# Kernel optimization log

Measured on AMD Instinct MI355X. Metric: run time of the kernel, lower is better.

The kernel has to match this reference:

```python
import jax, jax.numpy as jnp
import numpy as np

D_MODEL = 1024
N_HEADS = 16
D_KV = 64
B, S = 2, 2048


def setup_inputs() -> dict:
    key = jax.random.key(0)
    ks = jax.random.split(key, 7)
    scale = 1.0 / np.sqrt(D_MODEL)
    return {
        "query": jax.random.normal(ks[0], (B, S, D_MODEL), jnp.float32),
        "key": jax.random.normal(ks[1], (B, S, D_MODEL), jnp.float32),
        "value": jax.random.normal(ks[2], (B, S, D_MODEL), jnp.float32),
        "mask": jnp.zeros((B, 1, 1, S), jnp.float32),
        "Wq": jax.random.normal(ks[3], (D_MODEL, N_HEADS * D_KV), jnp.float32) * scale,
        "Wk": jax.random.normal(ks[4], (D_MODEL, N_HEADS * D_KV), jnp.float32) * scale,
        "Wv": jax.random.normal(ks[5], (D_MODEL, N_HEADS * D_KV), jnp.float32) * scale,
        "Wo": jax.random.normal(ks[6], (N_HEADS * D_KV, D_MODEL), jnp.float32) * scale,
    }


def _split_heads(x):
    b, s, _ = x.shape
    return x.reshape(b, s, N_HEADS, D_KV).transpose(0, 2, 1, 3)  # [B,H,S,Dk]


def reference(query, key, value, mask, Wq, Wk, Wv, Wo):
    q = _split_heads(query @ Wq)
    k = _split_heads(key @ Wk)
    v = _split_heads(value @ Wv)
    scores = jnp.einsum("bhqd,bhkd->bhqk", q, k) / jnp.sqrt(
        jnp.asarray(D_KV, scores_dtype := q.dtype)
    )
    scores = scores + mask
    attn = jax.nn.softmax(scores, axis=-1)  # dropout_rate=0 -> identity
    ctx = jnp.einsum("bhqk,bhkd->bhqd", attn, v)
    ctx = ctx.transpose(0, 2, 1, 3).reshape(query.shape[0], -1, N_HEADS * D_KV)
    hidden = ctx @ Wo
    return hidden
```

## Files before the change

kernel.cpp:

```cpp
#include <hip/hip_runtime.h>
#include <hip/hip_bf16.h>
#include <stdint.h>

typedef __bf16 bf16;
typedef __bf16 bf16x8 __attribute__((ext_vector_type(8)));
typedef __bf16 bf16x4 __attribute__((ext_vector_type(4)));
typedef float  f32x4  __attribute__((ext_vector_type(4)));
typedef float  f32x16 __attribute__((ext_vector_type(16)));

#define S_LEN  2048
#define NH     16
#define DKV    64
#define DMODEL 1024
#define LOG2E  1.4426950408889634f

#define SBAR()       __builtin_amdgcn_s_barrier()
#define SFENCE()     __builtin_amdgcn_sched_barrier(0)
#define WAIT_VM(N)   asm volatile("s_waitcnt vmcnt(" #N ")" ::: "memory")
#define WAIT_LGKM0() asm volatile("s_waitcnt lgkmcnt(0)" ::: "memory")

__device__ __forceinline__ void async_load16(const void* g, void* l) {
  __builtin_amdgcn_global_load_lds(
      (const __attribute__((address_space(1))) uint32_t*)(uintptr_t)g,
      (__attribute__((address_space(3))) uint32_t*)(uintptr_t)l,
      16, 0, 0);
}

__global__ void prep(const float* __restrict__ W0, const float* __restrict__ W1,
                     const float* __restrict__ W2, const float* __restrict__ W3,
                     const float* __restrict__ Aq, const float* __restrict__ Ak,
                     const float* __restrict__ Av,
                     bf16* __restrict__ T0, bf16* __restrict__ T1,
                     bf16* __restrict__ T2, bf16* __restrict__ T3,
                     bf16* __restrict__ Qb, bf16* __restrict__ Kb, bf16* __restrict__ Vb)
{
  const int z = blockIdx.z;
  const int tid = threadIdx.x;
  if (z < 4) {
    if (blockIdx.x >= 16) return;
    const float* W = (z == 0) ? W0 : (z == 1) ? W1 : (z == 2) ? W2 : W3;
    bf16* T = (z == 0) ? T0 : (z == 1) ? T1 : (z == 2) ? T2 : T3;
    __shared__ float tile[64][65];
    int n0 = blockIdx.x * 64, k0 = blockIdx.y * 64;
    int c4 = (tid & 15) * 4;
    int rr = tid >> 4;
    for (int g = 0; g < 4; ++g) {
      int k = g * 16 + rr;
      f32x4 v = *(const f32x4*)(W + (size_t)(k0 + k) * DMODEL + n0 + c4);
      tile[k][c4] = v[0]; tile[k][c4 + 1] = v[1];
      tile[k][c4 + 2] = v[2]; tile[k][c4 + 3] = v[3];
    }
    __syncthreads();
    int kc = tid & 7, rn2 = tid >> 3;
    for (int pass = 0; pass < 2; ++pass) {
      int rn = pass * 32 + rn2;
      bf16x8 o;
      for (int w = 0; w < 8; ++w) o[w] = (bf16)tile[kc * 8 + w][rn];
      *(bf16x8*)(T + (size_t)(n0 + rn) * DMODEL + k0 + kc * 8) = o;
    }
  } else {
    const float* S = (z == 4) ? Aq : (z == 5) ? Ak : Av;
    bf16* D = (z == 4) ? Qb : (z == 5) ? Kb : Vb;
    size_t base = (((size_t)blockIdx.y * 64 + blockIdx.x) * 256 + tid) * 16;
    f32x4 v0 = *(const f32x4*)(S + base);
    f32x4 v1 = *(const f32x4*)(S + base + 4);
    f32x4 v2 = *(const f32x4*)(S + base + 8);
    f32x4 v3 = *(const f32x4*)(S + base + 12);
    bf16x8 o0, o1;
    for (int w = 0; w < 4; ++w) { o0[w] = (bf16)v0[w]; o0[w + 4] = (bf16)v1[w]; }
    for (int w = 0; w < 4; ++w) { o1[w] = (bf16)v2[w]; o1[w + 4] = (bf16)v3[w]; }
    *(bf16x8*)(D + base) = o0;
    *(bf16x8*)(D + base + 8) = o1;
  }
}

__global__ __launch_bounds__(256) void gemm_qkv(
    const bf16* __restrict__ Aq, const bf16* __restrict__ Ak, const bf16* __restrict__ Av,
    const bf16* __restrict__ Bq, const bf16* __restrict__ Bk, const bf16* __restrict__ Bv,
    bf16* __restrict__ Cq, bf16* __restrict__ Ck, bf16* __restrict__ Cv)
{
  __shared__ __align__(16) char smem[33792];
  bf16* As = (bf16*)smem;
  bf16* Bs = (bf16*)(smem + 16384);
  bf16* Ls = (bf16*)smem;

  const int z = blockIdx.z;
  const bf16* A  = (z == 0) ? Aq : (z == 1) ? Ak : Av;
  const bf16* Bt = (z == 0) ? Bq : (z == 1) ? Bk : Bv;
  bf16* C        = (z == 0) ? Cq : (z == 1) ? Ck : Cv;

  const int m0 = blockIdx.x * 128;
  const int n0 = blockIdx.y * 128;
  const int tid = threadIdx.x;
  const int lane = tid & 63;
  const int wave = tid >> 6;
  const int wm = (wave >> 1) * 64;
  const int wn = (wave & 1) * 64;
  const int row = lane & 15;
  const int quad = lane >> 4;

  f32x4 acc[4][4];
  for (int i = 0; i < 4; ++i)
    for (int j = 0; j < 4; ++j) acc[i][j] = (f32x4){0.f, 0.f, 0.f, 0.f};

  for (int kt = 0; kt < 16; ++kt) {
    const int kk = kt << 6;
    for (int j = 0; j < 4; ++j) {
      int base = j * 256 + wave * 64;
      int idx = base + lane;
      int r = idx >> 3;
      int cc = (idx & 7) ^ (r & 7);
      async_load16(A  + (size_t)(m0 + r) * DMODEL + kk + cc * 8,
                   (char*)As + (size_t)base * 16);
      async_load16(Bt + (size_t)(n0 + r) * DMODEL + kk + cc * 8,
                   (char*)Bs + (size_t)base * 16);
    }
    WAIT_VM(0);
    SBAR();
    for (int ks = 0; ks < 2; ++ks) {
      bf16x8 af[4], bfr[4];
      for (int i = 0; i < 4; ++i) {
        int rr = wm + i * 16 + row;
        af[i] = *(const bf16x8*)(As + rr * 64 + (((quad + ks * 4) ^ (rr & 7)) << 3));
      }
      for (int j = 0; j < 4; ++j) {
        int rr = wn + j * 16 + row;
        bfr[j] = *(const bf16x8*)(Bs + rr * 64 + (((quad + ks * 4) ^ (rr & 7)) << 3));
      }
      for (int i = 0; i < 4; ++i)
        for (int j = 0; j < 4; ++j)
          acc[i][j] = __builtin_amdgcn_mfma_f32_16x16x32_bf16(af[i], bfr[j], acc[i][j], 0, 0, 0);
    }
    SBAR();
  }

  if (z != 2) {
    const int bq = m0 >> 11;
    __syncthreads();
    for (int i = 0; i < 4; ++i)
      for (int j = 0; j < 4; ++j)
        for (int r = 0; r < 4; ++r)
          Ls[(wm + i * 16 + quad * 4 + r) * 132 + wn + j * 16 + row] = (bf16)acc[i][j][r];
    __syncthreads();
    for (int u = 0; u < 8; ++u) {
      int cc = u * 256 + tid;
      int rloc = cc >> 4, c8 = (cc & 15) * 8;
      int s = (m0 + rloc) & 2047;
      int gn = n0 + c8;
      int h = gn >> 6, d = gn & 63;
      bf16x8 val = *(const bf16x8*)(Ls + rloc * 132 + c8);
      *(bf16x8*)(C + (((size_t)(bq * NH + h)) * S_LEN + s) * DKV + d) = val;
    }
  } else {
    for (int i = 0; i < 4; ++i)
      for (int j = 0; j < 4; ++j) {
        int gm = m0 + wm + i * 16 + quad * 4;
        int gn = n0 + wn + j * 16 + row;
        int b = gm >> 11, s = gm & 2047;
        int h = gn >> 6,  d = gn & 63;
        int bh = b * NH + h;
        int tile = s >> 6, kb = (s & 63) >> 2;
        int half = (kb >> 1) & 1;
        int p = (kb & 1) + ((kb >> 2) & 1) * 2 + (kb >> 3) * 4;
        bf16x4 t;
        for (int r = 0; r < 4; ++r) t[r] = (bf16)acc[i][j][r];
        *(bf16x4*)(C + ((((size_t)bh * 32 + tile) * 8 + p) * 64 + d) * 8 + half * 4) = t;
      }
  }
}

__global__ __launch_bounds__(256, 4) void attn_kernel(
    const bf16* __restrict__ Qh, const bf16* __restrict__ Kh, const bf16* __restrict__ Vperm,
    const float* __restrict__ mask, bf16* __restrict__ Opart, float* __restrict__ Lpart)
{
  __shared__ __align__(16) bf16 Ks[2][64 * 64];
  __shared__ __align__(16) bf16 Vts[2][64 * 64];
  __shared__ __align__(16) float masks2[2][64];

  const int bh = blockIdx.x;
  const int b = bh >> 4;
  const int q0 = blockIdx.y * 128;
  const int zh = blockIdx.z;
  const int tid = threadIdx.x;
  const int lane = tid & 63;
  const int wave = tid >> 6;
  const int ln = lane & 31;
  const int hi = lane >> 5;
  const float SC2 = 0.125f * LOG2E;

  const int qg = q0 + wave * 32 + ln;
  bf16x8 qf[4];
  {
    const bf16* qrow = Qh + ((size_t)bh * S_LEN + qg) * DKV;
    for (int c = 0; c < 4; ++c)
      qf[c] = *(const bf16x8*)(qrow + c * 16 + hi * 8);
  }

  auto stage = [&](int it, int buf) {
    const int kv0 = zh * 1024 + it * 64;
    float mval = 0.f;
    if (tid < 64) mval = mask[b * S_LEN + kv0 + tid];
    const bf16* vtile = Vperm + ((size_t)bh * 32 + (kv0 >> 6)) * 4096;
    for (int j = 0; j < 2; ++j) {
      int base = j * 256 + wave * 64;
      int idx = base + lane;
      int r = idx >> 3;
      int cc = (idx & 7) ^ (r & 7);
      async_load16(Kh + ((size_t)bh * S_LEN + kv0 + r) * DKV + cc * 8,
                   (char*)Ks[buf] + (size_t)base * 16);
      async_load16(vtile + (size_t)idx * 8,
                   (char*)Vts[buf] + (size_t)base * 16);
    }
    if (tid < 64) masks2[buf][tid] = mval * LOG2E;
  };

  f32x16 O[2];
  for (int nb = 0; nb < 2; ++nb)
    for (int i = 0; i < 16; ++i) O[nb][i] = 0.f;
  float lsum = 0.f;

  stage(0, 0);

  for (int it = 0; it < 16; ++it) {
    const int cur = it & 1;
    if (it < 15) stage(it + 1, cur ^ 1);
    SFENCE();
    if (it < 15) { WAIT_VM(4); }
    else         { WAIT_VM(0); }
    WAIT_LGKM0();
    SBAR();
    SFENCE();

    f32x16 Sm[2];
    for (int i = 0; i < 16; ++i) { Sm[0][i] = 0.f; Sm[1][i] = 0.f; }
    __builtin_amdgcn_s_setprio(1);
    for (int c = 0; c < 4; ++c) {
      bf16x8 k0 = *(const bf16x8*)(Ks[cur] + ln * 64        + (((2 * c + hi) ^ (ln & 7)) << 3));
      bf16x8 k1 = *(const bf16x8*)(Ks[cur] + (32 + ln) * 64 + (((2 * c + hi) ^ (ln & 7)) << 3));
      Sm[0] = __builtin_amdgcn_mfma_f32_32x32x16_bf16(k0, qf[c], Sm[0], 0, 0, 0);
      Sm[1] = __builtin_amdgcn_mfma_f32_32x32x16_bf16(k1, qf[c], Sm[1], 0, 0, 0);
    }
    __builtin_amdgcn_s_setprio(0);

    for (int cg = 0; cg < 4; ++cg) {
      int mb = cg >> 1, g = cg & 1;
      int koff = 32 * mb + 16 * g + 4 * hi;
      f32x4 mklo = *(const f32x4*)(&masks2[cur][koff]);
      f32x4 mkhi = *(const f32x4*)(&masks2[cur][koff + 8]);
      bf16x8 ap;
      float ls0 = 0.f;
      for (int u = 0; u < 4; ++u) {
        float p = __builtin_amdgcn_exp2f(Sm[mb][g * 8 + u] * SC2 + mklo[u]);
        ls0 += p; ap[u] = (bf16)p;
      }
      for (int u = 0; u < 4; ++u) {
        float p = __builtin_amdgcn_exp2f(Sm[mb][g * 8 + 4 + u] * SC2 + mkhi[u]);
        ls0 += p; ap[4 + u] = (bf16)p;
      }
      lsum += ls0;
      int p = hi + 2 * g + 4 * mb;
      __builtin_amdgcn_s_setprio(1);
      for (int nb = 0; nb < 2; ++nb) {
        int d = nb * 32 + ln;
        bf16x8 bv = *(const bf16x8*)(Vts[cur] + ((size_t)p * 64 + d) * 8);
        O[nb] = __builtin_amdgcn_mfma_f32_32x32x16_bf16(ap, bv, O[nb], 0, 0, 0);
      }
      __builtin_amdgcn_s_setprio(0);
    }
    SFENCE();
    SBAR();
  }

  float lt = lsum + __shfl_xor(lsum, 32, 64);
  if (lane < 32)
    Lpart[((size_t)zh * 32 + bh) * S_LEN + q0 + wave * 32 + ln] = lt;

  bf16* ob = Opart + (((size_t)zh * 32 + bh) * S_LEN) * DKV;
  for (int g = 0; g < 4; ++g)
    for (int nb = 0; nb < 2; ++nb)
      for (int j = 0; j < 4; ++j) {
        int qrow = q0 + wave * 32 + j + 8 * g + 4 * hi;
        ob[(size_t)qrow * DKV + nb * 32 + ln] = (bf16)O[nb][g * 4 + j];
      }
}

__global__ __launch_bounds__(256) void gemm_out(
    const bf16* __restrict__ Opart, const float* __restrict__ Lpart,
    const bf16* __restrict__ Wot, float* __restrict__ Cout)
{
  __shared__ __align__(16) bf16 As[64 * 64];
  __shared__ __align__(16) bf16 Bs[2][128 * 64];
  __shared__ float rinv[NH * 64];

  const int m0 = blockIdx.x * 64;
  const int n0 = blockIdx.y * 128;
  const int tid = threadIdx.x;
  const int lane = tid & 63;
  const int wave = tid >> 6;
  const int wm = (wave >> 1) * 32;
  const int wn = (wave & 1) * 64;
  const int row = lane & 15;
  const int quad = lane >> 4;
  const int b = m0 >> 11;
  const int s0 = m0 & 2047;

  for (int u = 0; u < 4; ++u) {
    int idx = u * 256 + tid;
    int h = idx >> 6, r = idx & 63;
    float l = Lpart[(size_t)(b * NH + h) * S_LEN + s0 + r]
            + Lpart[(size_t)(32 + b * NH + h) * S_LEN + s0 + r];
    rinv[idx] = 1.0f / l;
  }
  SFENCE();

  f32x4 acc[2][4];
  for (int i = 0; i < 2; ++i)
    for (int j = 0; j < 4; ++j) acc[i][j] = (f32x4){0.f, 0.f, 0.f, 0.f};

  const int arc = tid & 7;
  const int arr = tid >> 3;
  const size_t HSTEP = (size_t)S_LEN * DKV;
  const size_t ZSTEP = (size_t)32 * S_LEN * DKV;
  const bf16* Oa = Opart + ((size_t)(b * NH) * S_LEN + s0 + arr) * DKV + arc * 8;
  const bf16* Ob = Oa + (size_t)32 * DKV;

  auto stageB = [&](int kt, int buf) {
    for (int j = 0; j < 4; ++j) {
      int base = j * 256 + wave * 64;
      int idx = base + lane;
      int r = idx >> 3;
      int cc = (idx & 7) ^ (r & 7);
      async_load16(Wot + (size_t)(n0 + r) * DMODEL + kt * 64 + cc * 8,
                   (char*)Bs[buf] + (size_t)base * 16);
    }
  };

  bf16x8 h00 = *(const bf16x8*)(Oa);
  bf16x8 h01 = *(const bf16x8*)(Oa + ZSTEP);
  bf16x8 h10 = *(const bf16x8*)(Ob);
  bf16x8 h11 = *(const bf16x8*)(Ob + ZSTEP);
  SFENCE();
  stageB(0, 0);
  SFENCE();
  WAIT_LGKM0();
  SBAR();

  for (int kt = 0; kt < 16; ++kt) {
    const int cur = kt & 1;
    if (kt < 15) stageB(kt + 1, cur ^ 1);
    {
      float rv  = rinv[kt * 64 + arr];
      float rv2 = rinv[kt * 64 + 32 + arr];
      bf16x8 o;
      for (int w = 0; w < 8; ++w)
        o[w] = (bf16)(((float)h00[w] + (float)h01[w]) * rv);
      *(bf16x8*)(As + arr * 64 + ((arc ^ (arr & 7)) << 3)) = o;
      for (int w = 0; w < 8; ++w)
        o[w] = (bf16)(((float)h10[w] + (float)h11[w]) * rv2);
      *(bf16x8*)(As + (32 + arr) * 64 + ((arc ^ (arr & 7)) << 3)) = o;
    }
    if (kt < 15) {
      const size_t off = (size_t)(kt + 1) * HSTEP;
      h00 = *(const bf16x8*)(Oa + off);
      h01 = *(const bf16x8*)(Oa + off + ZSTEP);
      h10 = *(const bf16x8*)(Ob + off);
      h11 = *(const bf16x8*)(Ob + off + ZSTEP);
    }
    SFENCE();
    if (kt < 15) { WAIT_VM(8); }
    else         { WAIT_VM(0); }
    WAIT_LGKM0();
    SBAR();
    SFENCE();
    for (int ks = 0; ks < 2; ++ks) {
      bf16x8 af[2], bfr[4];
      for (int i = 0; i < 2; ++i) {
        int rr = wm + i * 16 + row;
        af[i] = *(const bf16x8*)(As + rr * 64 + (((quad + ks * 4) ^ (rr & 7)) << 3));
      }
      for (int j = 0; j < 4; ++j) {
        int rr = wn + j * 16 + row;
        bfr[j] = *(const bf16x8*)(Bs[cur] + rr * 64 + (((quad + ks * 4) ^ (rr & 7)) << 3));
      }
      for (int i = 0; i < 2; ++i)
        for (int j = 0; j < 4; ++j)
          acc[i][j] = __builtin_amdgcn_mfma_f32_16x16x32_bf16(af[i], bfr[j], acc[i][j], 0, 0, 0);
    }
    SFENCE();
    SBAR();
  }

  for (int i = 0; i < 2; ++i)
    for (int j = 0; j < 4; ++j)
      for (int r = 0; r < 4; ++r) {
        int gm = m0 + wm + i * 16 + quad * 4 + r;
        int gn = n0 + wn + j * 16 + row;
        Cout[(size_t)gm * DMODEL + gn] = acc[i][j][r];
      }
}

extern "C" void kernel_launch(void* const* d_in, const int* in_sizes, int n_in,
                              void* d_out, int out_size, void* d_ws, size_t ws_size,
                              hipStream_t stream)
{
  const float* query = (const float*)d_in[0];
  const float* key_  = (const float*)d_in[1];
  const float* value = (const float*)d_in[2];
  const float* mask  = (const float*)d_in[3];
  const float* Wq = (const float*)d_in[4];
  const float* Wk = (const float*)d_in[5];
  const float* Wv = (const float*)d_in[6];
  const float* Wo = (const float*)d_in[7];

  char* ws = (char*)d_ws;
  const size_t MB = (size_t)1 << 20;
  bf16* qh    = (bf16*)(ws + 0 * MB);
  bf16* kh    = (bf16*)(ws + 8 * MB);
  bf16* vperm = (bf16*)(ws + 16 * MB);
  bf16* wot   = (bf16*)(ws + 24 * MB);
  bf16* Opart = (bf16*)(ws + 26 * MB);
  bf16* wqt   = (bf16*)(ws + 26 * MB);
  bf16* wkt   = (bf16*)(ws + 28 * MB);
  bf16* wvt   = (bf16*)(ws + 30 * MB);
  bf16* qb    = (bf16*)(ws + 32 * MB);
  bf16* kb    = (bf16*)(ws + 40 * MB);
  bf16* vb    = (bf16*)(ws + 48 * MB);
  float* Lpart = (float*)(ws + 58 * MB);

  prep<<<dim3(64, 16, 7), 256, 0, stream>>>(Wq, Wk, Wv, Wo, query, key_, value,
                                            wqt, wkt, wvt, wot, qb, kb, vb);
  gemm_qkv<<<dim3(32, 8, 3), 256, 0, stream>>>(qb, kb, vb, wqt, wkt, wvt,
                                               qh, kh, vperm);
  attn_kernel<<<dim3(32, 16, 2), 256, 0, stream>>>(qh, kh, vperm, mask, Opart, Lpart);
  gemm_out<<<dim3(64, 8), 256, 0, stream>>>(Opart, Lpart, wot, (float*)d_out);
}
```

Measured before the change: 218.2 us.

## Drop split-KV in attention, normalize in-kernel and write contiguous ctx

The attention kernel stops splitting the KV range into two halves. Each block now walks all 32 KV tiles, normalizes by the row sum itself, and writes a bf16 context in [B,S,D] layout. The output GEMM then loads A tiles asynchronously like B, without merging partials or rescaling, and the setprio hints are removed. This halves the attention grid (512 blocks instead of 1024) and lengthens each block, trading fewer blocks for less partial traffic and a simpler output GEMM.

```diff
diff --git a/kernel.cpp b/kernel.cpp
--- a/kernel.cpp
+++ b/kernel.cpp
@@ -171,16 +171,16 @@
 
 __global__ __launch_bounds__(256, 4) void attn_kernel(
     const bf16* __restrict__ Qh, const bf16* __restrict__ Kh, const bf16* __restrict__ Vperm,
-    const float* __restrict__ mask, bf16* __restrict__ Opart, float* __restrict__ Lpart)
+    const float* __restrict__ mask, bf16* __restrict__ ctx)
 {
   __shared__ __align__(16) bf16 Ks[2][64 * 64];
   __shared__ __align__(16) bf16 Vts[2][64 * 64];
   __shared__ __align__(16) float masks2[2][64];
+  __shared__ float lrow[128];
 
   const int bh = blockIdx.x;
   const int b = bh >> 4;
   const int q0 = blockIdx.y * 128;
-  const int zh = blockIdx.z;
   const int tid = threadIdx.x;
   const int lane = tid & 63;
   const int wave = tid >> 6;
@@ -197,10 +197,10 @@
   }
 
   auto stage = [&](int it, int buf) {
-    const int kv0 = zh * 1024 + it * 64;
+    const int kv0 = it * 64;
     float mval = 0.f;
     if (tid < 64) mval = mask[b * S_LEN + kv0 + tid];
-    const bf16* vtile = Vperm + ((size_t)bh * 32 + (kv0 >> 6)) * 4096;
+    const bf16* vtile = Vperm + ((size_t)bh * 32 + it) * 4096;
     for (int j = 0; j < 2; ++j) {
       int base = j * 256 + wave * 64;
       int idx = base + lane;
@@ -221,11 +221,11 @@
 
   stage(0, 0);
 
-  for (int it = 0; it < 16; ++it) {
+  for (int it = 0; it < 32; ++it) {
     const int cur = it & 1;
-    if (it < 15) stage(it + 1, cur ^ 1);
-    SFENCE();
-    if (it < 15) { WAIT_VM(4); }
+    if (it < 31) stage(it + 1, cur ^ 1);
+    SFENCE();
+    if (it < 31) { WAIT_VM(4); }
     else         { WAIT_VM(0); }
     WAIT_LGKM0();
     SBAR();
@@ -233,14 +233,12 @@
 
     f32x16 Sm[2];
     for (int i = 0; i < 16; ++i) { Sm[0][i] = 0.f; Sm[1][i] = 0.f; }
-    __builtin_amdgcn_s_setprio(1);
     for (int c = 0; c < 4; ++c) {
       bf16x8 k0 = *(const bf16x8*)(Ks[cur] + ln * 64        + (((2 * c + hi) ^ (ln & 7)) << 3));
       bf16x8 k1 = *(const bf16x8*)(Ks[cur] + (32 + ln) * 64 + (((2 * c + hi) ^ (ln & 7)) << 3));
       Sm[0] = __builtin_amdgcn_mfma_f32_32x32x16_bf16(k0, qf[c], Sm[0], 0, 0, 0);
       Sm[1] = __builtin_amdgcn_mfma_f32_32x32x16_bf16(k1, qf[c], Sm[1], 0, 0, 0);
     }
-    __builtin_amdgcn_s_setprio(0);
 
     for (int cg = 0; cg < 4; ++cg) {
       int mb = cg >> 1, g = cg & 1;
@@ -259,38 +257,36 @@
       }
       lsum += ls0;
       int p = hi + 2 * g + 4 * mb;
-      __builtin_amdgcn_s_setprio(1);
       for (int nb = 0; nb < 2; ++nb) {
         int d = nb * 32 + ln;
         bf16x8 bv = *(const bf16x8*)(Vts[cur] + ((size_t)p * 64 + d) * 8);
         O[nb] = __builtin_amdgcn_mfma_f32_32x32x16_bf16(ap, bv, O[nb], 0, 0, 0);
       }
-      __builtin_amdgcn_s_setprio(0);
     }
     SFENCE();
     SBAR();
   }
 
   float lt = lsum + __shfl_xor(lsum, 32, 64);
-  if (lane < 32)
-    Lpart[((size_t)zh * 32 + bh) * S_LEN + q0 + wave * 32 + ln] = lt;
-
-  bf16* ob = Opart + (((size_t)zh * 32 + bh) * S_LEN) * DKV;
+  if (hi == 0) lrow[wave * 32 + ln] = 1.0f / lt;
+  __syncthreads();
+
+  const int hcol = (bh & 15) * DKV;
   for (int g = 0; g < 4; ++g)
-    for (int nb = 0; nb < 2; ++nb)
-      for (int j = 0; j < 4; ++j) {
-        int qrow = q0 + wave * 32 + j + 8 * g + 4 * hi;
-        ob[(size_t)qrow * DKV + nb * 32 + ln] = (bf16)O[nb][g * 4 + j];
-      }
+    for (int j = 0; j < 4; ++j) {
+      int qrl = wave * 32 + j + 8 * g + 4 * hi;
+      float sc = lrow[qrl];
+      for (int nb = 0; nb < 2; ++nb)
+        ctx[((size_t)(b * S_LEN + q0 + qrl)) * DMODEL + hcol + nb * 32 + ln]
+          = (bf16)(O[nb][g * 4 + j] * sc);
+    }
 }
 
 __global__ __launch_bounds__(256) void gemm_out(
-    const bf16* __restrict__ Opart, const float* __restrict__ Lpart,
-    const bf16* __restrict__ Wot, float* __restrict__ Cout)
-{
-  __shared__ __align__(16) bf16 As[64 * 64];
+    const bf16* __restrict__ Ctx, const bf16* __restrict__ Wot, float* __restrict__ Cout)
+{
+  __shared__ __align__(16) bf16 As[2][64 * 64];
   __shared__ __align__(16) bf16 Bs[2][128 * 64];
-  __shared__ float rinv[NH * 64];
 
   const int m0 = blockIdx.x * 64;
   const int n0 = blockIdx.y * 128;
@@ -301,82 +297,46 @@
   const int wn = (wave & 1) * 64;
   const int row = lane & 15;
   const int quad = lane >> 4;
-  const int b = m0 >> 11;
-  const int s0 = m0 & 2047;
-
-  for (int u = 0; u < 4; ++u) {
-    int idx = u * 256 + tid;
-    int h = idx >> 6, r = idx & 63;
-    float l = Lpart[(size_t)(b * NH + h) * S_LEN + s0 + r]
-            + Lpart[(size_t)(32 + b * NH + h) * S_LEN + s0 + r];
-    rinv[idx] = 1.0f / l;
-  }
-  SFENCE();
 
   f32x4 acc[2][4];
   for (int i = 0; i < 2; ++i)
     for (int j = 0; j < 4; ++j) acc[i][j] = (f32x4){0.f, 0.f, 0.f, 0.f};
 
-  const int arc = tid & 7;
-  const int arr = tid >> 3;
-  const size_t HSTEP = (size_t)S_LEN * DKV;
-  const size_t ZSTEP = (size_t)32 * S_LEN * DKV;
-  const bf16* Oa = Opart + ((size_t)(b * NH) * S_LEN + s0 + arr) * DKV + arc * 8;
-  const bf16* Ob = Oa + (size_t)32 * DKV;
-
-  auto stageB = [&](int kt, int buf) {
+  auto stage = [&](int kt, int buf) {
+    const int kk = kt << 6;
+    for (int j = 0; j < 2; ++j) {
+      int base = j * 256 + wave * 64;
+      int idx = base + lane;
+      int r = idx >> 3;
+      int cc = (idx & 7) ^ (r & 7);
+      async_load16(Ctx + (size_t)(m0 + r) * DMODEL + kk + cc * 8,
+                   (char*)As[buf] + (size_t)base * 16);
+    }
     for (int j = 0; j < 4; ++j) {
       int base = j * 256 + wave * 64;
       int idx = base + lane;
       int r = idx >> 3;
       int cc = (idx & 7) ^ (r & 7);
-      async_load16(Wot + (size_t)(n0 + r) * DMODEL + kt * 64 + cc * 8,
+      async_load16(Wot + (size_t)(n0 + r) * DMODEL + kk + cc * 8,
                    (char*)Bs[buf] + (size_t)base * 16);
     }
   };
 
-  bf16x8 h00 = *(const bf16x8*)(Oa);
-  bf16x8 h01 = *(const bf16x8*)(Oa + ZSTEP);
-  bf16x8 h10 = *(const bf16x8*)(Ob);
-  bf16x8 h11 = *(const bf16x8*)(Ob + ZSTEP);
-  SFENCE();
-  stageB(0, 0);
-  SFENCE();
-  WAIT_LGKM0();
-  SBAR();
+  stage(0, 0);
 
   for (int kt = 0; kt < 16; ++kt) {
     const int cur = kt & 1;
-    if (kt < 15) stageB(kt + 1, cur ^ 1);
-    {
-      float rv  = rinv[kt * 64 + arr];
-      float rv2 = rinv[kt * 64 + 32 + arr];
-      bf16x8 o;
-      for (int w = 0; w < 8; ++w)
-        o[w] = (bf16)(((float)h00[w] + (float)h01[w]) * rv);
-      *(bf16x8*)(As + arr * 64 + ((arc ^ (arr & 7)) << 3)) = o;
-      for (int w = 0; w < 8; ++w)
-        o[w] = (bf16)(((float)h10[w] + (float)h11[w]) * rv2);
-      *(bf16x8*)(As + (32 + arr) * 64 + ((arc ^ (arr & 7)) << 3)) = o;
-    }
-    if (kt < 15) {
-      const size_t off = (size_t)(kt + 1) * HSTEP;
-      h00 = *(const bf16x8*)(Oa + off);
-      h01 = *(const bf16x8*)(Oa + off + ZSTEP);
-      h10 = *(const bf16x8*)(Ob + off);
-      h11 = *(const bf16x8*)(Ob + off + ZSTEP);
-    }
-    SFENCE();
-    if (kt < 15) { WAIT_VM(8); }
+    if (kt < 15) stage(kt + 1, cur ^ 1);
+    SFENCE();
+    if (kt < 15) { WAIT_VM(6); }
     else         { WAIT_VM(0); }
-    WAIT_LGKM0();
     SBAR();
     SFENCE();
     for (int ks = 0; ks < 2; ++ks) {
       bf16x8 af[2], bfr[4];
       for (int i = 0; i < 2; ++i) {
         int rr = wm + i * 16 + row;
-        af[i] = *(const bf16x8*)(As + rr * 64 + (((quad + ks * 4) ^ (rr & 7)) << 3));
+        af[i] = *(const bf16x8*)(As[cur] + rr * 64 + (((quad + ks * 4) ^ (rr & 7)) << 3));
       }
       for (int j = 0; j < 4; ++j) {
         int rr = wn + j * 16 + row;
@@ -418,19 +378,18 @@
   bf16* kh    = (bf16*)(ws + 8 * MB);
   bf16* vperm = (bf16*)(ws + 16 * MB);
   bf16* wot   = (bf16*)(ws + 24 * MB);
-  bf16* Opart = (bf16*)(ws + 26 * MB);
-  bf16* wqt   = (bf16*)(ws + 26 * MB);
-  bf16* wkt   = (bf16*)(ws + 28 * MB);
-  bf16* wvt   = (bf16*)(ws + 30 * MB);
-  bf16* qb    = (bf16*)(ws + 32 * MB);
-  bf16* kb    = (bf16*)(ws + 40 * MB);
-  bf16* vb    = (bf16*)(ws + 48 * MB);
-  float* Lpart = (float*)(ws + 58 * MB);
+  bf16* ctx   = (bf16*)(ws + 26 * MB);
+  bf16* wqt   = (bf16*)(ws + 34 * MB);
+  bf16* wkt   = (bf16*)(ws + 36 * MB);
+  bf16* wvt   = (bf16*)(ws + 38 * MB);
+  bf16* qb    = (bf16*)(ws + 40 * MB);
+  bf16* kb    = (bf16*)(ws + 48 * MB);
+  bf16* vb    = (bf16*)(ws + 56 * MB);
 
   prep<<<dim3(64, 16, 7), 256, 0, stream>>>(Wq, Wk, Wv, Wo, query, key_, value,
                                             wqt, wkt, wvt, wot, qb, kb, vb);
   gemm_qkv<<<dim3(32, 8, 3), 256, 0, stream>>>(qb, kb, vb, wqt, wkt, wvt,
                                                qh, kh, vperm);
-  attn_kernel<<<dim3(32, 16, 2), 256, 0, stream>>>(qh, kh, vperm, mask, Opart, Lpart);
-  gemm_out<<<dim3(64, 8), 256, 0, stream>>>(Opart, Lpart, wot, (float*)d_out);
-}
+  attn_kernel<<<dim3(32, 16), 256, 0, stream>>>(qh, kh, vperm, mask, ctx);
+  gemm_out<<<dim3(64, 8), 256, 0, stream>>>(ctx, wot, (float*)d_out);
+}
```

After: 209.7 us. 1.04x faster.
